# Kernel tuning notes

Hardware: AMD Instinct MI355X
Metric: run time of the kernel (lower is better)

The kernel has to match this reference:

```python
import jax, jax.numpy as jnp
import numpy as np

B, L, S, D, H = 4, 2048, 2048, 1024, 16
HD = D // H


def setup_inputs() -> dict:
    key = jax.random.key(0)
    ks = jax.random.split(key, 7)
    scale = 1.0 / np.sqrt(D)
    q = jax.random.normal(ks[0], (B, L, D), dtype=jnp.float32)
    k = jax.random.normal(ks[1], (B, S, D), dtype=jnp.float32)
    v = jax.random.normal(ks[2], (B, S, D), dtype=jnp.float32)
    # causal mask, broadcast over batch and heads; 0 -> masked
    mask = jnp.tril(jnp.ones((L, S), dtype=jnp.int32))[None, None]
    Wq = jax.random.normal(ks[3], (D, D), dtype=jnp.float32) * scale
    Wk = jax.random.normal(ks[4], (D, D), dtype=jnp.float32) * scale
    Wv = jax.random.normal(ks[5], (D, D), dtype=jnp.float32) * scale
    Wo = jax.random.normal(ks[6], (D, D), dtype=jnp.float32) * scale
    return {"q": q, "k": k, "v": v, "mask": mask,
            "Wq": Wq, "Wk": Wk, "Wv": Wv, "Wo": Wo}


def reference(q, k, v, mask, Wq, Wk, Wv, Wo):
    Bq, Lq, _ = q.shape
    Sk = k.shape[1]
    # torch nn.Linear: y = x @ W.T  (W is [out, in])
    qh = (q @ Wq.T).reshape(Bq, Lq, H, HD).transpose(0, 2, 1, 3)  # [B,H,L,hd]
    kh = (k @ Wk.T).reshape(Bq, Sk, H, HD).transpose(0, 2, 1, 3)  # [B,H,S,hd]
    vh = (v @ Wv.T).reshape(Bq, Sk, H, HD).transpose(0, 2, 1, 3)  # [B,H,S,hd]
    scores = jnp.einsum('bhld,bhsd->bhls', qh, kh) / jnp.sqrt(jnp.float32(HD))
    scores = jnp.where(mask == 0, -jnp.inf, scores)
    attn = jax.nn.softmax(scores, axis=-1)
    out = jnp.einsum('bhls,bhsd->bhld', attn, vh)
    out = out.transpose(0, 2, 1, 3).reshape(Bq, Lq, D)
    return out @ Wo.T
```

## Files before the change

### kernel.cpp

```cpp
#include <hip/hip_runtime.h>
#include <hip/hip_bf16.h>

#define BB 4
#define LL 2048
#define SS 2048
#define DD 1024
#define HH 16
#define HD 64

typedef __bf16 bf16;
typedef __attribute__((ext_vector_type(8))) __bf16 bf16x8;
typedef __attribute__((ext_vector_type(4))) float f32x4;

#define ASYNC16(gp, lp)                                                        \
  __builtin_amdgcn_global_load_lds(                                            \
      (__attribute__((address_space(1))) void*)(gp),                           \
      (__attribute__((address_space(3))) void*)(lp), 16, 0, 0)

__global__ __launch_bounds__(256) void detect_dtype(
    const unsigned short* __restrict__ qbits, int* __restrict__ flag) {
  __shared__ int smax;
  if (threadIdx.x == 0) smax = 0;
  __syncthreads();
  int m = 0;
  for (int i = threadIdx.x; i < 4096; i += 256) {
    const int e = (qbits[i] >> 7) & 0xFF;
    m = m > e ? m : e;
  }
  atomicMax(&smax, m);
  __syncthreads();
  if (threadIdx.x == 0) *flag = (smax >= 0xC0) ? 1 : 0;
}

__global__ __launch_bounds__(256) void convert_all(
    const void* __restrict__ q, const void* __restrict__ k,
    const void* __restrict__ v, const void* __restrict__ Wq,
    const void* __restrict__ Wk, const void* __restrict__ Wv,
    const void* __restrict__ Wo, bf16* __restrict__ cq, bf16* __restrict__ ck,
    bf16* __restrict__ cv, bf16* __restrict__ cWq, bf16* __restrict__ cWk,
    bf16* __restrict__ cWv, bf16* __restrict__ cWo,
    const int* __restrict__ flag) {
  const int b = blockIdx.x;
  const void* src;
  bf16* dst;
  int lb;
  if (b < 12288) {
    const int t = b >> 12;
    lb = b & 4095;
    src = (t == 0) ? q : (t == 1) ? k : v;
    dst = (t == 0) ? cq : (t == 1) ? ck : cv;
  } else {
    const int t = (b - 12288) >> 9;
    lb = (b - 12288) & 511;
    src = (t == 0) ? Wq : (t == 1) ? Wk : (t == 2) ? Wv : Wo;
    dst = (t == 0) ? cWq : (t == 1) ? cWk : (t == 2) ? cWv : cWo;
  }
  const int i8 = (lb * 256 + threadIdx.x) * 8;
  if (*flag) {
    const float4* s = (const float4*)src;
    const float4 a = s[i8 / 4];
    const float4 c = s[i8 / 4 + 1];
    bf16x8 o;
    o[0] = (bf16)a.x; o[1] = (bf16)a.y; o[2] = (bf16)a.z; o[3] = (bf16)a.w;
    o[4] = (bf16)c.x; o[5] = (bf16)c.y; o[6] = (bf16)c.z; o[7] = (bf16)c.w;
    *(bf16x8*)(dst + i8) = o;
  } else {
    *(uint4*)(dst + i8) = ((const uint4*)src)[i8 / 8];
  }
}

#define GM 8192
#define GN 1024
#define GK 1024

#define GEMM_BODY(X, W)                                                        \
  const int tid = threadIdx.x;                                                 \
  const int lane = tid & 63;                                                   \
  const int wave = tid >> 6;                                                   \
  const int l15 = lane & 15;                                                   \
  const int quad = lane >> 4;                                                  \
  const int wm = wave >> 1;                                                    \
  const int wn = wave & 1;                                                     \
  const int lin = blockIdx.y * 8 + blockIdx.x;                                 \
  const int tileN = ((lin >> 3) & 7) * 128;                                    \
  const int tileM = ((lin & 7) | ((lin >> 6) << 3)) * 128;                     \
  __shared__ bf16 As[128 * 64];                                                \
  __shared__ bf16 Bs[128 * 64];                                                \
  f32x4 acc[4][4];                                                             \
  _Pragma("unroll") for (int mi = 0; mi < 4; ++mi)                             \
      _Pragma("unroll") for (int ni = 0; ni < 4; ++ni)                         \
          acc[mi][ni] = (f32x4){0.f, 0.f, 0.f, 0.f};                           \
  const int srow8 = lane >> 3;                                                 \
  const int jsw = (lane & 7) ^ srow8;                                          \
  const int swz8 = l15 & 7;                                                    \
  for (int k0 = 0; k0 < GK; k0 += 64) {                                        \
    __syncthreads();                                                           \
    _Pragma("unroll") for (int i = 0; i < 4; ++i) {                            \
      const int r0 = (i * 4 + wave) * 8;                                       \
      ASYNC16(X + (size_t)(tileM + r0 + srow8) * GK + k0 + jsw * 8,            \
              &As[r0 * 64]);                                                   \
      ASYNC16(W + (size_t)(tileN + r0 + srow8) * GK + k0 + jsw * 8,            \
              &Bs[r0 * 64]);                                                   \
    }                                                                          \
    __syncthreads();                                                           \
    _Pragma("unroll") for (int ks = 0; ks < 2; ++ks) {                         \
      bf16x8 a[4], b[4];                                                       \
      _Pragma("unroll") for (int mi = 0; mi < 4; ++mi)                         \
          a[mi] = *(const bf16x8*)&As[(wm * 64 + mi * 16 + l15) * 64 +         \
                                      (((ks * 4 + quad) ^ swz8) * 8)];         \
      _Pragma("unroll") for (int ni = 0; ni < 4; ++ni)                         \
          b[ni] = *(const bf16x8*)&Bs[(wn * 64 + ni * 16 + l15) * 64 +         \
                                      (((ks * 4 + quad) ^ swz8) * 8)];         \
      _Pragma("unroll") for (int mi = 0; mi < 4; ++mi)                         \
          _Pragma("unroll") for (int ni = 0; ni < 4; ++ni)                     \
              acc[mi][ni] = __builtin_amdgcn_mfma_f32_16x16x32_bf16(           \
                  a[mi], b[ni], acc[mi][ni], 0, 0, 0);                         \
    }                                                                          \
  }

__global__ __launch_bounds__(256, 3) void gemm_qkv(
    const bf16* __restrict__ cq, const bf16* __restrict__ ck,
    const bf16* __restrict__ cv, const bf16* __restrict__ cWq,
    const bf16* __restrict__ cWk, const bf16* __restrict__ cWv,
    bf16* __restrict__ qh, bf16* __restrict__ kh, bf16* __restrict__ vt) {
  const int z = blockIdx.z;
  const bf16* X = (z == 0) ? cq : (z == 1) ? ck : cv;
  const bf16* W = (z == 0) ? cWq : (z == 1) ? cWk : cWv;
  bf16* Out = (z == 0) ? qh : (z == 1) ? kh : vt;
  GEMM_BODY(X, W)
#pragma unroll
  for (int mi = 0; mi < 4; ++mi)
#pragma unroll
    for (int ni = 0; ni < 4; ++ni)
#pragma unroll
      for (int r = 0; r < 4; ++r) {
        const int row = tileM + wm * 64 + mi * 16 + quad * 4 + r;
        const int col = tileN + wn * 64 + ni * 16 + l15;
        const int b_ = row >> 11;
        const int l_ = row & 2047;
        const int h_ = col >> 6;
        const int hd_ = col & 63;
        size_t idx;
        if (z < 2)
          idx = (((size_t)(b_ * HH + h_)) * LL + l_) * HD + hd_;
        else
          idx = (((size_t)(b_ * HH + h_)) * HD + hd_) * SS + l_;
        Out[idx] = (bf16)acc[mi][ni][r];
      }
}

__global__ __launch_bounds__(256, 3) void gemm_out(const bf16* __restrict__ X,
                                                   const bf16* __restrict__ W,
                                                   void* __restrict__ Outv,
                                                   const int* __restrict__ flag) {
  GEMM_BODY(X, W)
  const bool f32out = (*flag != 0);
#pragma unroll
  for (int mi = 0; mi < 4; ++mi)
#pragma unroll
    for (int ni = 0; ni < 4; ++ni)
#pragma unroll
      for (int r = 0; r < 4; ++r) {
        const int row = tileM + wm * 64 + mi * 16 + quad * 4 + r;
        const int col = tileN + wn * 64 + ni * 16 + l15;
        const size_t idx = (size_t)row * GN + col;
        if (f32out)
          ((float*)Outv)[idx] = acc[mi][ni][r];
        else
          ((bf16*)Outv)[idx] = (bf16)acc[mi][ni][r];
      }
}

#define PS_STRIDE 72

__global__ __launch_bounds__(256, 4) void attn_fwd(const bf16* __restrict__ Qh,
                                                   const bf16* __restrict__ Kh,
                                                   const bf16* __restrict__ Vt,
                                                   bf16* __restrict__ AOut) {
  const int tid = threadIdx.x;
  const int lane = tid & 63;
  const int wave = tid >> 6;
  const int l15 = lane & 15;
  const int quad = lane >> 4;

  const int bh = blockIdx.y;
  const int b_ = bh >> 4;
  const int h_ = bh & 15;

  const bf16* Qb = Qh + (size_t)bh * LL * HD;
  const bf16* Kb = Kh + (size_t)bh * SS * HD;
  const bf16* Vb = Vt + (size_t)bh * HD * SS;

  __shared__ bf16 Ks[64 * 64];
  __shared__ bf16 Vs[64 * 64];
  __shared__ bf16 Ps[4][16 * PS_STRIDE];

  bf16x8 onef;
#pragma unroll
  for (int j = 0; j < 8; ++j) onef[j] = (l15 == 0) ? (bf16)1.0f : (bf16)0.0f;

  const int srow8 = lane >> 3;
  const int jsw = (lane & 7) ^ srow8;
  const int swz = l15 & 7;

  for (int ph = 0; ph < 2; ++ph) {
    const int qt = ph ? (31 - blockIdx.x) : blockIdx.x;
    const int qrow0 = qt * 64 + wave * 16;

    bf16x8 qf[2];
#pragma unroll
    for (int ks = 0; ks < 2; ++ks)
      qf[ks] =
          *(const bf16x8*)(Qb + (size_t)(qrow0 + l15) * HD + ks * 32 + quad * 8);

    f32x4 o[5];
#pragma unroll
    for (int ni = 0; ni < 5; ++ni) o[ni] = (f32x4){0.f, 0.f, 0.f, 0.f};

    for (int st = 0; st <= qt; ++st) {
      const int s0 = st * 64;
      __syncthreads();
#pragma unroll
      for (int i = 0; i < 2; ++i) {
        const int r0 = (i * 4 + wave) * 8;
        ASYNC16(Kb + (size_t)(s0 + r0 + srow8) * HD + jsw * 8, &Ks[r0 * 64]);
        ASYNC16(Vb + (size_t)(r0 + srow8) * SS + s0 + jsw * 8, &Vs[r0 * 64]);
      }
      __syncthreads();

      f32x4 sc[4];
#pragma unroll
      for (int ni = 0; ni < 4; ++ni) {
        sc[ni] = (f32x4){0.f, 0.f, 0.f, 0.f};
#pragma unroll
        for (int ks = 0; ks < 2; ++ks) {
          bf16x8 kf = *(const bf16x8*)&Ks[(ni * 16 + l15) * 64 +
                                          (((ks * 4 + quad) ^ swz) * 8)];
          sc[ni] = __builtin_amdgcn_mfma_f32_16x16x32_bf16(qf[ks], kf, sc[ni],
                                                           0, 0, 0);
        }
      }

      if (st < qt) {
#pragma unroll
        for (int ni = 0; ni < 4; ++ni)
#pragma unroll
          for (int r = 0; r < 4; ++r) {
            const float p = __expf(fmaf(sc[ni][r], 0.125f, -12.0f));
            Ps[wave][(quad * 4 + r) * PS_STRIDE + ni * 16 + l15] = (bf16)p;
          }
      } else {
#pragma unroll
        for (int ni = 0; ni < 4; ++ni) {
          const int scolg = s0 + ni * 16 + l15;
#pragma unroll
          for (int r = 0; r < 4; ++r) {
            const int qrow = qrow0 + quad * 4 + r;
            const float p = (scolg <= qrow)
                                ? __expf(fmaf(sc[ni][r], 0.125f, -12.0f))
                                : 0.f;
            Ps[wave][(quad * 4 + r) * PS_STRIDE + ni * 16 + l15] = (bf16)p;
          }
        }
      }

#pragma unroll
      for (int ks = 0; ks < 2; ++ks) {
        bf16x8 pf =
            *(const bf16x8*)&Ps[wave][l15 * PS_STRIDE + ks * 32 + quad * 8];
#pragma unroll
        for (int ni = 0; ni < 4; ++ni) {
          bf16x8 vf = *(const bf16x8*)&Vs[(ni * 16 + l15) * 64 +
                                          (((ks * 4 + quad) ^ swz) * 8)];
          o[ni] =
              __builtin_amdgcn_mfma_f32_16x16x32_bf16(pf, vf, o[ni], 0, 0, 0);
        }
        o[4] = __builtin_amdgcn_mfma_f32_16x16x32_bf16(pf, onef, o[4], 0, 0, 0);
      }
    }

#pragma unroll
    for (int r = 0; r < 4; ++r) {
      const float l = __shfl(o[4][r], lane & 48);
      const float inv = 1.f / l;
      const int row = qrow0 + quad * 4 + r;
#pragma unroll
      for (int ni = 0; ni < 4; ++ni) {
        AOut[((size_t)(b_ * LL + row)) * DD + h_ * HD + ni * 16 + l15] =
            (bf16)(o[ni][r] * inv);
      }
    }
  }
}

extern "C" void kernel_launch(void* const* d_in, const int* in_sizes, int n_in,
                              void* d_out, int out_size, void* d_ws,
                              size_t ws_size, hipStream_t stream) {
  (void)in_sizes; (void)n_in; (void)out_size; (void)ws_size;
  const void* q = d_in[0];
  const void* k = d_in[1];
  const void* v = d_in[2];
  const void* Wq = d_in[4];
  const void* Wk = d_in[5];
  const void* Wv = d_in[6];
  const void* Wo = d_in[7];

  const size_t Sq = (size_t)BB * LL * DD;
  const size_t Sw = (size_t)DD * DD;

  int* flag = (int*)d_ws;
  bf16* base = (bf16*)((char*)d_ws + 16);
  bf16* cq = base;
  bf16* ck = cq + Sq;
  bf16* cv = ck + Sq;
  bf16* cWq = cv + Sq;
  bf16* cWk = cWq + Sw;
  bf16* cWv = cWk + Sw;
  bf16* cWo = cWv + Sw;
  bf16* qh = cWo + Sw;
  bf16* kh = qh + Sq;
  bf16* vt = kh + Sq;
  bf16* ao = vt + Sq;

  dim3 blk(256);
  detect_dtype<<<1, blk, 0, stream>>>((const unsigned short*)q, flag);
  convert_all<<<14336, blk, 0, stream>>>(q, k, v, Wq, Wk, Wv, Wo, cq, ck, cv,
                                         cWq, cWk, cWv, cWo, flag);
  gemm_qkv<<<dim3(GN / 128, GM / 128, 3), blk, 0, stream>>>(cq, ck, cv, cWq,
                                                            cWk, cWv, qh, kh,
                                                            vt);
  attn_fwd<<<dim3(16, BB * HH), blk, 0, stream>>>(qh, kh, vt, ao);
  gemm_out<<<dim3(GN / 128, GM / 128), blk, 0, stream>>>(ao, cWo, d_out, flag);
}
```

Before: 354.0 us.

## Triple-buffer GEMM tiles with async prefetch and enlarge to 256x128 blocks

Result: slower. 371.7 us (+5.0%).

```diff
diff --git a/kernel.cpp b/kernel.cpp
--- a/kernel.cpp
+++ b/kernel.cpp
@@ -72,6 +72,25 @@
 #define GM 8192
 #define GN 1024
 #define GK 1024
+#define BM 256
+#define BN 128
+#define BK 64
+#define NKT (GK / BK)
+
+#define STAGE(bi, kt)                                                          \
+  do {                                                                         \
+    const int kk0_ = (kt) * BK;                                                \
+    _Pragma("unroll") for (int i_ = 0; i_ < 4; ++i_) {                         \
+      const int r0_ = (i_ * 8 + wave) * 8;                                     \
+      ASYNC16(X + (size_t)(tileM + r0_ + srow8) * GK + kk0_ + jsw * 8,         \
+              &As[bi][r0_ * 64]);                                              \
+    }                                                                          \
+    _Pragma("unroll") for (int i_ = 0; i_ < 2; ++i_) {                         \
+      const int r0_ = (i_ * 8 + wave) * 8;                                     \
+      ASYNC16(W + (size_t)(tileN + r0_ + srow8) * GK + kk0_ + jsw * 8,         \
+              &Bs[bi][r0_ * 64]);                                              \
+    }                                                                          \
+  } while (0)
 
 #define GEMM_BODY(X, W)                                                        \
   const int tid = threadIdx.x;                                                 \
@@ -79,13 +98,13 @@
   const int wave = tid >> 6;                                                   \
   const int l15 = lane & 15;                                                   \
   const int quad = lane >> 4;                                                  \
-  const int wm = wave >> 1;                                                    \
-  const int wn = wave & 1;                                                     \
+  const int wm = wave >> 1;                            \
+  const int wn = wave & 1;                             \
   const int lin = blockIdx.y * 8 + blockIdx.x;                                 \
-  const int tileN = ((lin >> 3) & 7) * 128;                                    \
-  const int tileM = ((lin & 7) | ((lin >> 6) << 3)) * 128;                     \
-  __shared__ bf16 As[128 * 64];                                                \
-  __shared__ bf16 Bs[128 * 64];                                                \
+  const int tileN = ((lin >> 3) & 7) * BN;                                     \
+  const int tileM = ((lin & 7) | ((lin >> 6) << 3)) * BM;                      \
+  __shared__ bf16 As[3][BM * BK];                                              \
+  __shared__ bf16 Bs[3][BN * BK];                                              \
   f32x4 acc[4][4];                                                             \
   _Pragma("unroll") for (int mi = 0; mi < 4; ++mi)                             \
       _Pragma("unroll") for (int ni = 0; ni < 4; ++ni)                         \
@@ -93,32 +112,45 @@
   const int srow8 = lane >> 3;                                                 \
   const int jsw = (lane & 7) ^ srow8;                                          \
   const int swz8 = l15 & 7;                                                    \
-  for (int k0 = 0; k0 < GK; k0 += 64) {                                        \
-    __syncthreads();                                                           \
-    _Pragma("unroll") for (int i = 0; i < 4; ++i) {                            \
-      const int r0 = (i * 4 + wave) * 8;                                       \
-      ASYNC16(X + (size_t)(tileM + r0 + srow8) * GK + k0 + jsw * 8,            \
-              &As[r0 * 64]);                                                   \
-      ASYNC16(W + (size_t)(tileN + r0 + srow8) * GK + k0 + jsw * 8,            \
-              &Bs[r0 * 64]);                                                   \
-    }                                                                          \
-    __syncthreads();                                                           \
+  STAGE(0, 0);                                                                 \
+  STAGE(1, 1);                                                                 \
+  asm volatile("s_waitcnt vmcnt(6)" ::: "memory");          \
+  __builtin_amdgcn_s_barrier();                                                \
+  int rb = 0, sb = 2;                                                          \
+  for (int t = 0; t < NKT; ++t) {                                              \
+    const bf16* Abuf = &As[rb][0];                                             \
+    const bf16* Bbuf = &Bs[rb][0];                                             \
     _Pragma("unroll") for (int ks = 0; ks < 2; ++ks) {                         \
       bf16x8 a[4], b[4];                                                       \
       _Pragma("unroll") for (int mi = 0; mi < 4; ++mi)                         \
-          a[mi] = *(const bf16x8*)&As[(wm * 64 + mi * 16 + l15) * 64 +         \
-                                      (((ks * 4 + quad) ^ swz8) * 8)];         \
+          a[mi] = *(const bf16x8*)&Abuf[(wm * 64 + mi * 16 + l15) * 64 +       \
+                                        (((ks * 4 + quad) ^ swz8) * 8)];       \
       _Pragma("unroll") for (int ni = 0; ni < 4; ++ni)                         \
-          b[ni] = *(const bf16x8*)&Bs[(wn * 64 + ni * 16 + l15) * 64 +         \
-                                      (((ks * 4 + quad) ^ swz8) * 8)];         \
+          b[ni] = *(const bf16x8*)&Bbuf[(wn * 64 + ni * 16 + l15) * 64 +       \
+                                        (((ks * 4 + quad) ^ swz8) * 8)];       \
+      if (ks == 0 && t + 2 < NKT) STAGE(sb, t + 2);                            \
+      __builtin_amdgcn_s_barrier();                                            \
+      __builtin_amdgcn_s_setprio(1);                                           \
       _Pragma("unroll") for (int mi = 0; mi < 4; ++mi)                         \
           _Pragma("unroll") for (int ni = 0; ni < 4; ++ni)                     \
               acc[mi][ni] = __builtin_amdgcn_mfma_f32_16x16x32_bf16(           \
                   a[mi], b[ni], acc[mi][ni], 0, 0, 0);                         \
+      __builtin_amdgcn_s_setprio(0);                                           \
+      if (ks == 0) {                                                           \
+        __builtin_amdgcn_s_barrier();                                          \
+      } else {                                                                 \
+        if (t + 2 < NKT)         \
+          asm volatile("s_waitcnt vmcnt(6)" ::: "memory");                     \
+        else if (t + 1 < NKT)         \
+          asm volatile("s_waitcnt vmcnt(0)" ::: "memory");                     \
+        __builtin_amdgcn_s_barrier();                                          \
+      }                                                                        \
     }                                                                          \
-  }
-
-__global__ __launch_bounds__(256, 3) void gemm_qkv(
+    rb = (rb == 2) ? 0 : rb + 1;                                               \
+    sb = (sb == 2) ? 0 : sb + 1;                                               \
+  }
+
+__global__ __launch_bounds__(512, 2) void gemm_qkv(
     const bf16* __restrict__ cq, const bf16* __restrict__ ck,
     const bf16* __restrict__ cv, const bf16* __restrict__ cWq,
     const bf16* __restrict__ cWk, const bf16* __restrict__ cWv,
@@ -149,7 +181,7 @@
       }
 }
 
-__global__ __launch_bounds__(256, 3) void gemm_out(const bf16* __restrict__ X,
+__global__ __launch_bounds__(512, 2) void gemm_out(const bf16* __restrict__ X,
                                                    const bf16* __restrict__ W,
                                                    void* __restrict__ Outv,
                                                    const int* __restrict__ flag) {
@@ -322,13 +354,11 @@
   bf16* vt = kh + Sq;
   bf16* ao = vt + Sq;
 
-  dim3 blk(256);
-  detect_dtype<<<1, blk, 0, stream>>>((const unsigned short*)q, flag);
-  convert_all<<<14336, blk, 0, stream>>>(q, k, v, Wq, Wk, Wv, Wo, cq, ck, cv,
-                                         cWq, cWk, cWv, cWo, flag);
-  gemm_qkv<<<dim3(GN / 128, GM / 128, 3), blk, 0, stream>>>(cq, ck, cv, cWq,
-                                                            cWk, cWv, qh, kh,
-                                                            vt);
-  attn_fwd<<<dim3(16, BB * HH), blk, 0, stream>>>(qh, kh, vt, ao);
-  gemm_out<<<dim3(GN / 128, GM / 128), blk, 0, stream>>>(ao, cWo, d_out, flag);
-}
+  detect_dtype<<<1, dim3(256), 0, stream>>>((const unsigned short*)q, flag);
+  convert_all<<<14336, dim3(256), 0, stream>>>(q, k, v, Wq, Wk, Wv, Wo, cq, ck,
+                                               cv, cWq, cWk, cWv, cWo, flag);
+  gemm_qkv<<<dim3(8, 32, 3), dim3(512), 0, stream>>>(cq, ck, cv, cWq, cWk,
+                                                     cWv, qh, kh, vt);
+  attn_fwd<<<dim3(16, BB * HH), dim3(256), 0, stream>>>(qh, kh, vt, ao);
+  gemm_out<<<dim3(8, 32), dim3(512), 0, stream>>>(ao, cWo, d_out, flag);
+}
```
